# Kernel optimization log

Hardware: AMD Instinct MI355X
Metric: run time of the kernel (lower is better)

Reference implementation:

```python
import jax, jax.numpy as jnp
import numpy as np

# Dimensions (see shape_source)
IN_VEC = 131072          # input_vector_size
NUM_CAPS = 512           # num_capsules (output capsules)
CAP_SIZE = 256           # capsule_size
RF_SIZE = 64             # receptive_field_size
RF_PER_CAP = CAP_SIZE // RF_SIZE        # 4
IN_CAPS = IN_VEC // CAP_SIZE            # 512 input_eff_capsules
CONN_P = 0.1             # connection_probability


def setup_inputs() -> dict:
    key = jax.random.key(0)
    kx, kc, kw = jax.random.split(key, 3)
    x = jax.random.normal(kx, (IN_VEC,), dtype=jnp.float32)
    # Sparse ScRRAMBLe routing tensor: mostly zeros, gated by connection probability.
    # Shape (input_eff_capsules, rf_per_cap_in, num_capsules, rf_per_cap_out) per einsum 'ijkl,ijm->klm'.
    Ci = (jax.random.uniform(kc, (IN_CAPS, RF_PER_CAP, NUM_CAPS, RF_PER_CAP)) < CONN_P).astype(jnp.float32)
    # glorot_normal over last two axes: fan_in = fan_out = RF_SIZE -> std = sqrt(2/(64+64)) = 0.125
    glorot_std = float(np.sqrt(2.0 / (RF_SIZE + RF_SIZE)))
    Wi = glorot_std * jax.random.normal(kw, (NUM_CAPS, RF_PER_CAP, RF_PER_CAP, RF_SIZE, RF_SIZE), dtype=jnp.float32)
    return {"x": x, "Ci": Ci, "Wi": Wi}


def reference(x, Ci, Wi):
    # x: (IN_VEC,) -> (input_eff_capsules, rf_per_cap, rf_size)
    x_reshaped = x.reshape(IN_CAPS, RF_PER_CAP, RF_SIZE)
    # Route input receptive fields to output capsule slots:
    # x_routed: (num_capsules, rf_per_cap, rf_size)
    x_routed = jnp.einsum('ijkl,ijm->klm', Ci, x_reshaped)
    # Per-capsule small batched transform:
    # y: (num_capsules, rf_per_cap, rf_size)
    y = jnp.einsum('ijklm,ikm->ijl', Wi, x_routed)
    return y
```

## Files before the change

kernel.cpp:

```cpp
#include <hip/hip_runtime.h>


typedef float f4 __attribute__((ext_vector_type(4)));

#define NCH 8

__global__ __launch_bounds__(256) void route_kernel(
    const float* __restrict__ x,
    const float* __restrict__ Ci,
    float* __restrict__ xr_part)
{
    const int iq  = blockIdx.x;
    const int c   = blockIdx.y;
    const int t   = threadIdx.x;
    const int il  = t >> 6;
    const int g   = (t >> 4) & 3;
    const int mq4 = t & 15;
    const int i   = (iq << 2) + il;

    const f4* __restrict__ Ci4 = (const f4*)Ci;
    const f4* __restrict__ x4  = (const f4*)x;

    __shared__ f4 part[1024];

    f4 a0 = {0.f,0.f,0.f,0.f};
    f4 a1 = {0.f,0.f,0.f,0.f};
    f4 a2 = {0.f,0.f,0.f,0.f};
    f4 a3 = {0.f,0.f,0.f,0.f};

    const int ijpc = 2048 / NCH;
    const int sub  = ijpc >> 2;
    const int base = c * ijpc + g * sub;
    #pragma unroll 4
    for (int it = 0; it < sub; ++it) {
        const int ij = base + it;
        const f4 c4 = Ci4[ij * 512 + i];
        const f4 xv = x4[(ij << 4) + mq4];
        a0 += c4.x * xv;
        a1 += c4.y * xv;
        a2 += c4.z * xv;
        a3 += c4.w * xv;
    }

    const int pb = ((g << 2) + il) << 2;
    part[(pb + 0) * 16 + mq4] = a0;
    part[(pb + 1) * 16 + mq4] = a1;
    part[(pb + 2) * 16 + mq4] = a2;
    part[(pb + 3) * 16 + mq4] = a3;
    __syncthreads();

    const int il2 = t >> 6;
    const int r   = (t >> 4) & 3;
    const int mm  = t & 15;
    f4 s = {0.f,0.f,0.f,0.f};
    #pragma unroll
    for (int gg = 0; gg < 4; ++gg)
        s += part[(((gg << 2) + il2) * 4 + r) * 16 + mm];

    f4* __restrict__ xp4 = (f4*)xr_part;
    xp4[(c * 512 + (iq << 2) + il2) * 64 + r * 16 + mm] = s;
}

__global__ __launch_bounds__(256) void reduce_xr_kernel(
    const float* __restrict__ xr_part,
    float* __restrict__ xr)
{
    const int t = blockIdx.x * 256 + threadIdx.x;
    const f4* __restrict__ p4 = (const f4*)xr_part;
    f4 s = {0.f,0.f,0.f,0.f};
    #pragma unroll
    for (int c = 0; c < NCH; ++c) s += p4[c * 32768 + t];
    ((f4*)xr)[t] = s;
}

__global__ __launch_bounds__(256) void transform_stream(
    const float* __restrict__ Wi,
    const float* __restrict__ xr,
    float* __restrict__ y)
{
    const int tid  = blockIdx.x * 256 + threadIdx.x;
    const int m16  = threadIdx.x & 15;

    const f4* __restrict__ W4  = (const f4*)Wi;
    const f4* __restrict__ xr4 = (const f4*)xr;

    #pragma unroll 4
    for (int it = 0; it < 32; ++it) {
        const int idx = it * 262144 + tid;
        const f4 w = W4[idx];
        const int row = idx >> 4;
        const int i   = row >> 10;
        const int k   = (row >> 6) & 3;
        const f4 xv = xr4[i * 64 + k * 16 + m16];
        const f4 s4 = w * xv;
        float p = s4.x + s4.y + s4.z + s4.w;
        p += __shfl_xor(p, 1);
        p += __shfl_xor(p, 2);
        p += __shfl_xor(p, 4);
        p += __shfl_xor(p, 8);
        if (m16 == 0) {
            const int yi = ((row >> 8) << 6) | (row & 63);
            atomicAdd(&y[yi], p);
        }
    }
}

extern "C" void kernel_launch(void* const* d_in, const int* in_sizes, int n_in,
                              void* d_out, int out_size, void* d_ws, size_t ws_size,
                              hipStream_t stream) {
    const float* x  = (const float*)d_in[0];
    const float* Ci = (const float*)d_in[1];
    const float* Wi = (const float*)d_in[2];
    float* y       = (float*)d_out;
    float* xr_part = (float*)d_ws;
    float* xr      = (float*)d_ws + NCH * 512 * 256;

    hipMemsetAsync(y, 0, (size_t)out_size * sizeof(float), stream);
    route_kernel<<<dim3(128, NCH), 256, 0, stream>>>(x, Ci, xr_part);
    reduce_xr_kernel<<<128, 256, 0, stream>>>(xr_part, xr);
    transform_stream<<<1024, 256, 0, stream>>>(Wi, xr, y);
}
```

Baseline: 225.3 us.

## Restructure transform kernel to accumulate over k in registers and drop atomics

Each wavefront in the transform kernel now owns half of one (capsule, j) output row block. It loads the four k-slices of xr once and accumulates over k in registers instead of issuing an atomicAdd per k partial. Weight loads are software-pipelined through two register buffers to keep memory requests in flight. Outputs are written directly, which lets the hipMemsetAsync of y be removed. Register pressure rises from holding 16 f4 weight values plus the accumulators.

```diff
diff --git a/kernel.cpp b/kernel.cpp
--- a/kernel.cpp
+++ b/kernel.cpp
@@ -78,30 +78,61 @@
     const float* __restrict__ xr,
     float* __restrict__ y)
 {
-    const int tid  = blockIdx.x * 256 + threadIdx.x;
-    const int m16  = threadIdx.x & 15;
+    const int wid  = blockIdx.x * 4 + (threadIdx.x >> 6);
+    const int b    = wid >> 1;
+    const int h    = wid & 1;
+    const int lane = threadIdx.x & 63;
+    const int lq   = lane >> 4;
+    const int m16  = lane & 15;
+    const int i    = b >> 2;
 
-    const f4* __restrict__ W4  = (const f4*)Wi;
-    const f4* __restrict__ xr4 = (const f4*)xr;
+    const f4* __restrict__ W4 = (const f4*)Wi;
+    const f4* __restrict__ X4 = (const f4*)xr;
 
-    #pragma unroll 4
-    for (int it = 0; it < 32; ++it) {
-        const int idx = it * 262144 + tid;
-        const f4 w = W4[idx];
-        const int row = idx >> 4;
-        const int i   = row >> 10;
-        const int k   = (row >> 6) & 3;
-        const f4 xv = xr4[i * 64 + k * 16 + m16];
-        const f4 s4 = w * xv;
-        float p = s4.x + s4.y + s4.z + s4.w;
+    const f4 xk0 = X4[i * 64 +  0 + m16];
+    const f4 xk1 = X4[i * 64 + 16 + m16];
+    const f4 xk2 = X4[i * 64 + 32 + m16];
+    const f4 xk3 = X4[i * 64 + 48 + m16];
+
+    const int base = (b * 256 + h * 32) * 16 + lane;
+
+    f4 wa[8], wb[8];
+    #pragma unroll
+    for (int jj = 0; jj < 8; ++jj) wa[jj] = W4[base +    0 + jj * 64];
+    #pragma unroll
+    for (int jj = 0; jj < 8; ++jj) wb[jj] = W4[base + 1024 + jj * 64];
+
+    float acc[8];
+    #pragma unroll
+    for (int jj = 0; jj < 8; ++jj)
+        acc[jj] = wa[jj].x*xk0.x + wa[jj].y*xk0.y + wa[jj].z*xk0.z + wa[jj].w*xk0.w;
+
+    #pragma unroll
+    for (int jj = 0; jj < 8; ++jj) wa[jj] = W4[base + 2048 + jj * 64];
+
+    #pragma unroll
+    for (int jj = 0; jj < 8; ++jj)
+        acc[jj] += wb[jj].x*xk1.x + wb[jj].y*xk1.y + wb[jj].z*xk1.z + wb[jj].w*xk1.w;
+
+    #pragma unroll
+    for (int jj = 0; jj < 8; ++jj) wb[jj] = W4[base + 3072 + jj * 64];
+
+    #pragma unroll
+    for (int jj = 0; jj < 8; ++jj)
+        acc[jj] += wa[jj].x*xk2.x + wa[jj].y*xk2.y + wa[jj].z*xk2.z + wa[jj].w*xk2.w;
+
+    #pragma unroll
+    for (int jj = 0; jj < 8; ++jj)
+        acc[jj] += wb[jj].x*xk3.x + wb[jj].y*xk3.y + wb[jj].z*xk3.z + wb[jj].w*xk3.w;
+
+    #pragma unroll
+    for (int jj = 0; jj < 8; ++jj) {
+        float p = acc[jj];
         p += __shfl_xor(p, 1);
         p += __shfl_xor(p, 2);
         p += __shfl_xor(p, 4);
         p += __shfl_xor(p, 8);
-        if (m16 == 0) {
-            const int yi = ((row >> 8) << 6) | (row & 63);
-            atomicAdd(&y[yi], p);
-        }
+        if (m16 == 0) y[b * 64 + h * 32 + jj * 4 + lq] = p;
     }
 }
 
@@ -115,7 +146,6 @@
     float* xr_part = (float*)d_ws;
     float* xr      = (float*)d_ws + NCH * 512 * 256;
 
-    hipMemsetAsync(y, 0, (size_t)out_size * sizeof(float), stream);
     route_kernel<<<dim3(128, NCH), 256, 0, stream>>>(x, Ci, xr_part);
     reduce_xr_kernel<<<128, 256, 0, stream>>>(xr_part, xr);
     transform_stream<<<1024, 256, 0, stream>>>(Wi, xr, y);
```

New measurement: 228.7 us. Within noise of the previous version (+1.5%).
